# Kernel optimization log

Measured on AMD Instinct MI355X. Metric: run time of the kernel, lower is better.

The kernel has to match this reference:

```python
import jax, jax.numpy as jnp
import numpy as np

B, N, DIM = 8, 1024, 768
HEADS, HEAD_DIM = 12, 64
INNER = HEADS * HEAD_DIM  # 768
SCALE = HEAD_DIM ** -0.5


def setup_inputs() -> dict:
    key = jax.random.key(0)
    k1, k2, k3, k4 = jax.random.split(key, 4)
    x = jax.random.normal(k1, (B, N, DIM), dtype=jnp.float32)
    # nn.Linear weights, stored as (in, out) for x @ W
    w_qkv = jax.random.normal(k2, (DIM, 3 * INNER), dtype=jnp.float32) * (DIM ** -0.5)
    w_out = jax.random.normal(k3, (INNER, DIM), dtype=jnp.float32) * (INNER ** -0.5)
    b_out = jax.random.normal(k4, (DIM,), dtype=jnp.float32) * 0.02
    return {"x": x, "w_qkv": w_qkv, "w_out": w_out, "b_out": b_out}


def reference(x, w_qkv, w_out, b_out):
    qkv = jnp.einsum('bnd,de->bne', x, w_qkv)  # [B, N, 3*INNER]
    q, k, v = jnp.split(qkv, 3, axis=-1)
    # 'b n (h d) -> b h n d'
    def split_heads(t):
        return t.reshape(B, N, HEADS, HEAD_DIM).transpose(0, 2, 1, 3)
    q, k, v = split_heads(q), split_heads(k), split_heads(v)
    score = jnp.einsum('bhnd,bhmd->bhnm', q, k) * SCALE  # [B, H, N, N]
    # Faithful to torch nn.Softmax() with dim=None on a 4D tensor: legacy
    # behavior applies softmax over dim=1 (the HEADS axis), NOT the key axis.
    attention = jax.nn.softmax(score, axis=1)
    out = jnp.einsum('bhnm,bhmd->bhnd', attention, v)  # [B, H, N, D]
    out = out.transpose(0, 2, 1, 3).reshape(B, N, INNER)  # 'b h n d -> b n (h d)'
    return jnp.einsum('bne,ed->bnd', out, w_out) + b_out
```

## Files before the change

### kernel.cpp

```cpp
#include <hip/hip_runtime.h>

typedef float  f32x4  __attribute__((ext_vector_type(4)));
typedef short  bf16x8 __attribute__((ext_vector_type(8)));

#define MFMA16(a, b, c) __builtin_amdgcn_mfma_f32_16x16x32_bf16((a), (b), (c), 0, 0, 0)

#define GLL16(g, l) __builtin_amdgcn_global_load_lds(                      \
    (const __attribute__((address_space(1))) void*)(g),                    \
    (__attribute__((address_space(3))) void*)(l), 16, 0, 0)

__device__ __forceinline__ short f2bf(float f) {
    union { float f; unsigned u; } a; a.f = f;
    unsigned r = a.u + 0x7fffu + ((a.u >> 16) & 1u);
    return (short)(r >> 16);
}
__device__ __forceinline__ float bf2f(unsigned short u) {
    union { unsigned u; float f; } a; a.u = ((unsigned)u) << 16; return a.f;
}

#define Bb   8
#define Nn   1024
#define DIM  768
#define HH   12
#define HD   64
#define INNER 768
#define SCALE 0.125f
#define SCL2E 0.18033688011112042f

__global__ void cast_to_bf16(const float* __restrict__ in, short* __restrict__ out, int n4) {
    int i = blockIdx.x * 256 + threadIdx.x;
    if (i >= n4) return;
    float4 f = reinterpret_cast<const float4*>(in)[i];
    unsigned lo = (unsigned)(unsigned short)f2bf(f.x) | ((unsigned)(unsigned short)f2bf(f.y) << 16);
    unsigned hi = (unsigned)(unsigned short)f2bf(f.z) | ((unsigned)(unsigned short)f2bf(f.w) << 16);
    reinterpret_cast<uint2*>(out)[i] = make_uint2(lo, hi);
}

__global__ void transpose_cast(const float* __restrict__ w, short* __restrict__ wt,
                               int rows, int cols) {
    int idx = blockIdx.x * 256 + threadIdx.x;
    if (idx >= rows * cols) return;
    int c = idx / rows;
    int k = idx - c * rows;
    wt[idx] = f2bf(w[k * cols + c]);
}

template <int MODE>
__global__ __launch_bounds__(256, 2)
void gemm128(const short* __restrict__ A, const short* __restrict__ Bt, int K,
             short* __restrict__ qb, short* __restrict__ kb, short* __restrict__ vtb,
             float* __restrict__ outp, const float* __restrict__ bias) {
    __shared__ __align__(16) short As[128 * 40];
    __shared__ __align__(16) short Bs[128 * 40];

    const int tid  = threadIdx.x;
    const int lane = tid & 63, wv = tid >> 6;
    const int wrow = wv >> 1, wcol = wv & 1;
    const int quad = lane >> 4, l16 = lane & 15;
    const int m0 = blockIdx.y * 128, n0 = blockIdx.x * 128;

    const int srow = tid >> 1;
    const int soff = (tid & 1) * 16;

    f32x4 acc[4][4];
#pragma unroll
    for (int i = 0; i < 4; i++)
#pragma unroll
        for (int j = 0; j < 4; j++) acc[i][j] = (f32x4){0.f, 0.f, 0.f, 0.f};

    for (int kc = 0; kc < K; kc += 32) {
        const uint4 a0 = *reinterpret_cast<const uint4*>(A + (size_t)(m0 + srow) * K + kc + soff);
        const uint4 a1 = *reinterpret_cast<const uint4*>(A + (size_t)(m0 + srow) * K + kc + soff + 8);
        const uint4 b0 = *reinterpret_cast<const uint4*>(Bt + (size_t)(n0 + srow) * K + kc + soff);
        const uint4 b1 = *reinterpret_cast<const uint4*>(Bt + (size_t)(n0 + srow) * K + kc + soff + 8);
        __syncthreads();
        *reinterpret_cast<uint4*>(&As[srow * 40 + soff])     = a0;
        *reinterpret_cast<uint4*>(&As[srow * 40 + soff + 8]) = a1;
        *reinterpret_cast<uint4*>(&Bs[srow * 40 + soff])     = b0;
        *reinterpret_cast<uint4*>(&Bs[srow * 40 + soff + 8]) = b1;
        __syncthreads();

        bf16x8 af[4], bfr[4];
#pragma unroll
        for (int t = 0; t < 4; t++)
            af[t] = *reinterpret_cast<bf16x8*>(&As[(wrow * 64 + t * 16 + l16) * 40 + quad * 8]);
#pragma unroll
        for (int t = 0; t < 4; t++)
            bfr[t] = *reinterpret_cast<bf16x8*>(&Bs[(wcol * 64 + t * 16 + l16) * 40 + quad * 8]);
#pragma unroll
        for (int rt = 0; rt < 4; rt++)
#pragma unroll
            for (int ct = 0; ct < 4; ct++)
                acc[rt][ct] = MFMA16(af[rt], bfr[ct], acc[rt][ct]);
    }

#pragma unroll
    for (int rt = 0; rt < 4; rt++) {
#pragma unroll
        for (int ct = 0; ct < 4; ct++) {
            const int c = n0 + wcol * 64 + ct * 16 + l16;
#pragma unroll
            for (int reg = 0; reg < 4; reg++) {
                const int r = m0 + wrow * 64 + rt * 16 + quad * 4 + reg;
                const float v = acc[rt][ct][reg];
                if (MODE == 0) {
                    const int b = r >> 10, n = r & 1023;
                    const int which = (c >= 1536) ? 2 : (c >= 768 ? 1 : 0);
                    const int cc = c - which * 768;
                    const int h = cc >> 6, d = cc & 63;
                    const int bh = b * HH + h;
                    const short bv = f2bf(v);
                    if (which == 0)      qb[(bh << 16) + (n << 6) + d] = bv;
                    else if (which == 1) kb[(bh << 16) + (n << 6) + d] = bv;
                    else                 vtb[(bh << 16) + (d << 10) + n] = bv;
                } else {
                    outp[(size_t)r * 768 + c] = v + bias[c];
                }
            }
        }
    }
}

__global__ __launch_bounds__(512, 4)
void attn_den5(const short* __restrict__ qb, const short* __restrict__ kb,
               short* __restrict__ invp) {
    __shared__ __align__(16) short Qs[2][128 * 64];
    __shared__ __align__(16) short Ks[2][128 * 64];

    const int tid = threadIdx.x, lane = tid & 63, wv = tid >> 6;
    const int wrow = wv >> 2, wcol = wv & 3;
    const int quad = lane >> 4, l16 = lane & 15;
    const int bid = blockIdx.x;
    const int b = bid & 7;
    const int nmt = bid >> 3;
    const int n0 = (nmt >> 3) << 7;
    const int m0 = (nmt & 7) << 7;

    const int r8 = lane >> 3;
    const int gu = (lane & 7) ^ r8;
    const int qo0 = (n0 + wv * 8 + r8) * 64 + gu * 8;
    const int qo1 = qo0 + 64 * 64;
    const int ko0 = (m0 + wv * 8 + r8) * 64 + gu * 8;
    const int ko1 = ko0 + 64 * 64;
    const int lc0 = wv * 512;
    const int lc1 = 4096 + wv * 512;

    f32x4 den[4][2];
#pragma unroll
    for (int i = 0; i < 4; i++)
#pragma unroll
        for (int j = 0; j < 2; j++) den[i][j] = (f32x4){0.f, 0.f, 0.f, 0.f};
    const f32x4 z = (f32x4){0.f, 0.f, 0.f, 0.f};

    {
        const short* qh = qb + ((size_t)(b * HH) << 16);
        const short* kh = kb + ((size_t)(b * HH) << 16);
        GLL16(qh + qo0, &Qs[0][lc0]);
        GLL16(qh + qo1, &Qs[0][lc1]);
        GLL16(kh + ko0, &Ks[0][lc0]);
        GLL16(kh + ko1, &Ks[0][lc1]);
    }

    for (int h = 0; h < HH; h++) {
        asm volatile("s_waitcnt vmcnt(0)" ::: "memory");
        __syncthreads();
        if (h < HH - 1) {
            const int pn = (h + 1) & 1;
            const short* qh = qb + ((size_t)(b * HH + h + 1) << 16);
            const short* kh = kb + ((size_t)(b * HH + h + 1) << 16);
            GLL16(qh + qo0, &Qs[pn][lc0]);
            GLL16(qh + qo1, &Qs[pn][lc1]);
            GLL16(kh + ko0, &Ks[pn][lc0]);
            GLL16(kh + ko1, &Ks[pn][lc1]);
        }
        const int pb = h & 1;
        const int sw0 = (quad ^ (l16 & 7)) * 8;

        bf16x8 aq[4][2], bk[2][2];
#pragma unroll
        for (int t = 0; t < 4; t++) {
            const int row = wrow * 64 + t * 16 + l16;
            aq[t][0] = *reinterpret_cast<bf16x8*>(&Qs[pb][row * 64 + sw0]);
            aq[t][1] = *reinterpret_cast<bf16x8*>(&Qs[pb][row * 64 + (sw0 ^ 32)]);
        }
#pragma unroll
        for (int t = 0; t < 2; t++) {
            const int row = wcol * 32 + t * 16 + l16;
            bk[t][0] = *reinterpret_cast<bf16x8*>(&Ks[pb][row * 64 + sw0]);
            bk[t][1] = *reinterpret_cast<bf16x8*>(&Ks[pb][row * 64 + (sw0 ^ 32)]);
        }
#pragma unroll
        for (int nt = 0; nt < 4; nt++)
#pragma unroll
            for (int mt = 0; mt < 2; mt++) {
                f32x4 s = MFMA16(aq[nt][0], bk[mt][0], z);
                s = MFMA16(aq[nt][1], bk[mt][1], s);
#pragma unroll
                for (int r = 0; r < 4; r++)
                    den[nt][mt][r] += __builtin_amdgcn_exp2f(s[r] * SCL2E);
            }
    }

#pragma unroll
    for (int nt = 0; nt < 4; nt++)
#pragma unroll
        for (int mt = 0; mt < 2; mt++) {
            const int ntg = (n0 >> 4) + wrow * 4 + nt;
            const int mtg = (m0 >> 4) + wcol * 2 + mt;
            ushort4 o;
            o.x = (unsigned short)f2bf(1.0f / den[nt][mt][0]);
            o.y = (unsigned short)f2bf(1.0f / den[nt][mt][1]);
            o.z = (unsigned short)f2bf(1.0f / den[nt][mt][2]);
            o.w = (unsigned short)f2bf(1.0f / den[nt][mt][3]);
            *reinterpret_cast<ushort4*>(&invp[(((b * 64 + ntg) * 64 + mtg) * 64 + lane) * 4]) = o;
        }
}

__global__ __launch_bounds__(256, 4)
void attn_pv2(const short* __restrict__ qb, const short* __restrict__ kb,
              const short* __restrict__ vtb, const short* __restrict__ invp,
              short* __restrict__ attn_out) {
    __shared__ __align__(16) short Ks[2][32 * 72];
    __shared__ __align__(16) short Vs[2][64 * 40];
    __shared__ __align__(16) short Ps[4][32 * 40];

    const int tid = threadIdx.x, lane = tid & 63, wv = tid >> 6;
    const int quad = lane >> 4, l16 = lane & 15;
    const int bid = blockIdx.x;
    const int b = bid & 7;
    const int r = bid >> 3;
    const int n4 = r / 12;
    const int h = r - n4 * 12;
    const int nb = n4 << 7;
    const int bh = b * HH + h;

    bf16x8 aq[2][2];
#pragma unroll
    for (int nt = 0; nt < 2; nt++) {
        const short* qp = qb + (bh << 16) + ((nb + wv * 32 + nt * 16 + l16) << 6) + quad * 8;
        aq[nt][0] = *reinterpret_cast<const bf16x8*>(qp);
        aq[nt][1] = *reinterpret_cast<const bf16x8*>(qp + 32);
    }

    const f32x4 z = (f32x4){0.f, 0.f, 0.f, 0.f};
    f32x4 O[2][4];
#pragma unroll
    for (int nt = 0; nt < 2; nt++)
#pragma unroll
        for (int d = 0; d < 4; d++) O[nt][d] = z;

    const int krow = tid >> 3, koff = (tid & 7) * 8;
    const int vrow = tid >> 2, voff = (tid & 3) * 8;

    uint4 kreg = *reinterpret_cast<const uint4*>(kb + (bh << 16) + (krow << 6) + koff);
    uint4 vreg = *reinterpret_cast<const uint4*>(vtb + (bh << 16) + (vrow << 10) + voff);

    for (int it = 0; it < 32; it++) {
        const int p = it & 1;
        *reinterpret_cast<uint4*>(&Ks[p][krow * 72 + koff]) = kreg;
        *reinterpret_cast<uint4*>(&Vs[p][vrow * 40 + voff]) = vreg;
        __syncthreads();
        if (it < 31) {
            const int m1 = (it + 1) << 5;
            kreg = *reinterpret_cast<const uint4*>(kb + (bh << 16) + ((m1 + krow) << 6) + koff);
            vreg = *reinterpret_cast<const uint4*>(vtb + (bh << 16) + (vrow << 10) + m1 + voff);
        }
        const int m0 = it << 5;

#pragma unroll
        for (int mh = 0; mh < 2; mh++) {
            const bf16x8 k0 = *reinterpret_cast<bf16x8*>(&Ks[p][(mh * 16 + l16) * 72 + quad * 8]);
            const bf16x8 k1 = *reinterpret_cast<bf16x8*>(&Ks[p][(mh * 16 + l16) * 72 + quad * 8 + 32]);
            const int mt = (m0 >> 4) + mh;
#pragma unroll
            for (int nt = 0; nt < 2; nt++) {
                f32x4 s = MFMA16(aq[nt][0], k0, z);
                s = MFMA16(aq[nt][1], k1, s);
                const int ntg = (nb >> 4) + wv * 2 + nt;
                const ushort4 iv = *reinterpret_cast<const ushort4*>(
                    &invp[(((b * 64 + ntg) * 64 + mt) * 64 + lane) * 4]);
                Ps[wv][(nt * 16 + quad * 4 + 0) * 40 + mh * 16 + l16] = f2bf(__expf(s[0] * SCALE) * bf2f(iv.x));
                Ps[wv][(nt * 16 + quad * 4 + 1) * 40 + mh * 16 + l16] = f2bf(__expf(s[1] * SCALE) * bf2f(iv.y));
                Ps[wv][(nt * 16 + quad * 4 + 2) * 40 + mh * 16 + l16] = f2bf(__expf(s[2] * SCALE) * bf2f(iv.z));
                Ps[wv][(nt * 16 + quad * 4 + 3) * 40 + mh * 16 + l16] = f2bf(__expf(s[3] * SCALE) * bf2f(iv.w));
            }
        }
        __threadfence_block();

        bf16x8 pa[2];
#pragma unroll
        for (int nt = 0; nt < 2; nt++)
            pa[nt] = *reinterpret_cast<bf16x8*>(&Ps[wv][(nt * 16 + l16) * 40 + quad * 8]);
#pragma unroll
        for (int dch = 0; dch < 4; dch++) {
            const bf16x8 vf = *reinterpret_cast<bf16x8*>(&Vs[p][(dch * 16 + l16) * 40 + quad * 8]);
#pragma unroll
            for (int nt = 0; nt < 2; nt++)
                O[nt][dch] = MFMA16(pa[nt], vf, O[nt][dch]);
        }
    }

#pragma unroll
    for (int nt = 0; nt < 2; nt++)
#pragma unroll
        for (int dch = 0; dch < 4; dch++) {
            const int col = h * 64 + dch * 16 + l16;
#pragma unroll
            for (int reg = 0; reg < 4; reg++) {
                const int n = nb + wv * 32 + nt * 16 + quad * 4 + reg;
                attn_out[(size_t)((b << 10) + n) * 768 + col] = f2bf(O[nt][dch][reg]);
            }
        }
}

extern "C" void kernel_launch(void* const* d_in, const int* in_sizes, int n_in,
                              void* d_out, int out_size, void* d_ws, size_t ws_size,
                              hipStream_t stream) {
    const float* x     = (const float*)d_in[0];
    const float* w_qkv = (const float*)d_in[1];
    const float* w_out = (const float*)d_in[2];
    const float* b_out = (const float*)d_in[3];
    float* out = (float*)d_out;

    short* xb   = (short*)d_ws;
    short* wT1  = xb  + 8192 * 768;
    short* wT2  = wT1 + 2304 * 768;
    short* qb   = wT2 + 768 * 768;
    short* kb   = qb  + 96 * 65536;
    short* vtb  = kb  + 96 * 65536;
    short* attn = vtb + 96 * 65536;
    short* invp = attn + 8192 * 768;

    cast_to_bf16<<<6144, 256, 0, stream>>>(x, xb, (8192 * 768) / 4);
    transpose_cast<<<(2304 * 768) / 256, 256, 0, stream>>>(w_qkv, wT1, 768, 2304);
    transpose_cast<<<(768 * 768) / 256, 256, 0, stream>>>(w_out, wT2, 768, 768);

    gemm128<0><<<dim3(2304 / 128, 8192 / 128), 256, 0, stream>>>(
        xb, wT1, 768, qb, kb, vtb, nullptr, nullptr);

    attn_den5<<<512, 512, 0, stream>>>(qb, kb, invp);
    attn_pv2<<<768, 256, 0, stream>>>(qb, kb, vtb, invp, attn);

    gemm128<1><<<dim3(768 / 128, 8192 / 128), 256, 0, stream>>>(
        attn, wT2, 768, nullptr, nullptr, nullptr, out, b_out);
}
```

Measured before the change: 257.5 us.

## Double-buffer GEMM tiles via direct global-to-LDS loads with XOR swizzle

```diff
diff --git a/kernel.cpp b/kernel.cpp
--- a/kernel.cpp
+++ b/kernel.cpp
@@ -46,12 +46,12 @@
 }
 
 template <int MODE>
-__global__ __launch_bounds__(256, 2)
+__global__ __launch_bounds__(256, 4)
 void gemm128(const short* __restrict__ A, const short* __restrict__ Bt, int K,
              short* __restrict__ qb, short* __restrict__ kb, short* __restrict__ vtb,
              float* __restrict__ outp, const float* __restrict__ bias) {
-    __shared__ __align__(16) short As[128 * 40];
-    __shared__ __align__(16) short Bs[128 * 40];
+    __shared__ __align__(16) short As[2][128 * 32];
+    __shared__ __align__(16) short Bs[2][128 * 32];
 
     const int tid  = threadIdx.x;
     const int lane = tid & 63, wv = tid >> 6;
@@ -59,8 +59,11 @@
     const int quad = lane >> 4, l16 = lane & 15;
     const int m0 = blockIdx.y * 128, n0 = blockIdx.x * 128;
 
-    const int srow = tid >> 1;
-    const int soff = (tid & 1) * 16;
+    const int row64 = (wv << 4) + (lane >> 2);
+    const int gu = (lane & 3) ^ ((lane >> 3) & 3);
+    const size_t aoff = (size_t)(m0 + row64) * K + gu * 8;
+    const size_t boff = (size_t)(n0 + row64) * K + gu * 8;
+    const int lch = wv * 512;
 
     f32x4 acc[4][4];
 #pragma unroll
@@ -68,25 +71,34 @@
 #pragma unroll
         for (int j = 0; j < 4; j++) acc[i][j] = (f32x4){0.f, 0.f, 0.f, 0.f};
 
-    for (int kc = 0; kc < K; kc += 32) {
-        const uint4 a0 = *reinterpret_cast<const uint4*>(A + (size_t)(m0 + srow) * K + kc + soff);
-        const uint4 a1 = *reinterpret_cast<const uint4*>(A + (size_t)(m0 + srow) * K + kc + soff + 8);
-        const uint4 b0 = *reinterpret_cast<const uint4*>(Bt + (size_t)(n0 + srow) * K + kc + soff);
-        const uint4 b1 = *reinterpret_cast<const uint4*>(Bt + (size_t)(n0 + srow) * K + kc + soff + 8);
+    GLL16(A  + aoff,                   &As[0][lch]);
+    GLL16(A  + aoff + (size_t)64 * K,  &As[0][2048 + lch]);
+    GLL16(Bt + boff,                   &Bs[0][lch]);
+    GLL16(Bt + boff + (size_t)64 * K,  &Bs[0][2048 + lch]);
+
+    const int swo = (quad ^ ((l16 >> 1) & 3)) * 8;
+
+    const int NK = K >> 5;
+    for (int ks = 0; ks < NK; ks++) {
+        asm volatile("s_waitcnt vmcnt(0)" ::: "memory");
         __syncthreads();
-        *reinterpret_cast<uint4*>(&As[srow * 40 + soff])     = a0;
-        *reinterpret_cast<uint4*>(&As[srow * 40 + soff + 8]) = a1;
-        *reinterpret_cast<uint4*>(&Bs[srow * 40 + soff])     = b0;
-        *reinterpret_cast<uint4*>(&Bs[srow * 40 + soff + 8]) = b1;
-        __syncthreads();
+        if (ks + 1 < NK) {
+            const int pn = (ks + 1) & 1;
+            const int kc = (ks + 1) << 5;
+            GLL16(A  + aoff + kc,                  &As[pn][lch]);
+            GLL16(A  + aoff + (size_t)64 * K + kc, &As[pn][2048 + lch]);
+            GLL16(Bt + boff + kc,                  &Bs[pn][lch]);
+            GLL16(Bt + boff + (size_t)64 * K + kc, &Bs[pn][2048 + lch]);
+        }
+        const int pb = ks & 1;
 
         bf16x8 af[4], bfr[4];
 #pragma unroll
         for (int t = 0; t < 4; t++)
-            af[t] = *reinterpret_cast<bf16x8*>(&As[(wrow * 64 + t * 16 + l16) * 40 + quad * 8]);
+            af[t] = *reinterpret_cast<bf16x8*>(&As[pb][(wrow * 64 + t * 16 + l16) * 32 + swo]);
 #pragma unroll
         for (int t = 0; t < 4; t++)
-            bfr[t] = *reinterpret_cast<bf16x8*>(&Bs[(wcol * 64 + t * 16 + l16) * 40 + quad * 8]);
+            bfr[t] = *reinterpret_cast<bf16x8*>(&Bs[pb][(wcol * 64 + t * 16 + l16) * 32 + swo]);
 #pragma unroll
         for (int rt = 0; rt < 4; rt++)
 #pragma unroll
```

Result: no change. 257.4 us (-0.0%).
